# Performance work log

Measured on AMD Instinct MI355X. Metric: run time of the kernel, lower is better.

## Reference

```python
import jax, jax.numpy as jnp
import numpy as np

LEAK = 0.1
BN_EPS = 1e-3  # keras BatchNormalization default epsilon
H = 256        # LSTM hidden size


def _conv1d_same(x, k):
    # x: [B, T, Cin], k: [3, Cin, Cout] -> [B, T, Cout]
    return jax.lax.conv_general_dilated(x, k, (1,), 'SAME',
                                        dimension_numbers=('NWC', 'WIO', 'NWC'))


def _bn_leaky(x, gamma, beta, mean, var):
    y = (x - mean) * jax.lax.rsqrt(var + BN_EPS) * gamma + beta
    return jnp.where(y > 0, y, LEAK * y)


def _lstm_cell(x, h, c, W, U, b):
    # keras LSTMCell: gates ordered i, f, g(candidate), o
    z = x @ W + h @ U + b  # [B, 4H]
    i, f, g, o = jnp.split(z, 4, axis=-1)
    c_new = jax.nn.sigmoid(f) * c + jax.nn.sigmoid(i) * jnp.tanh(g)
    h_new = jax.nn.sigmoid(o) * jnp.tanh(c_new)
    return h_new, c_new


def setup_inputs() -> dict:
    key = jax.random.key(0)
    ks = jax.random.split(key, 16)
    B, T = 128, 1024
    d = {}
    d['imu'] = jax.random.normal(ks[0], (B, T, 6), dtype=jnp.float32)
    # conv encoder params (no bias)
    chans = [(6, 64), (64, 128), (128, 256)]
    for li, (cin, cout) in enumerate(chans, start=1):
        d[f'k{li}'] = jax.random.normal(ks[li], (3, cin, cout), jnp.float32) * (1.0 / np.sqrt(3 * cin))
        d[f'g{li}'] = jnp.ones((cout,), jnp.float32)
        d[f'b{li}'] = jnp.zeros((cout,), jnp.float32)
        d[f'm{li}'] = jax.random.normal(ks[li + 3], (cout,), jnp.float32) * 0.05
        d[f'v{li}'] = jax.random.uniform(ks[li + 6], (cout,), jnp.float32) + 0.5
    # stacked LSTM params (2 layers of 256 units)
    for li, kidx in [(1, 10), (2, 13)]:
        d[f'W{li}'] = jax.random.normal(ks[kidx], (H, 4 * H), jnp.float32) * (1.0 / np.sqrt(H))
        d[f'U{li}'] = jax.random.normal(ks[kidx + 1], (H, 4 * H), jnp.float32) * (1.0 / np.sqrt(H))
        d[f'bl{li}'] = jnp.zeros((4 * H,), jnp.float32)
    return d


def reference(imu, k1, g1, b1, m1, v1, k2, g2, b2, m2, v2, k3, g3, b3, m3, v3,
              W1, U1, bl1, W2, U2, bl2):
    # Conv1D-BN-LeakyReLU encoder (inference-mode BN, training=False)
    x = _bn_leaky(_conv1d_same(imu, k1), g1, b1, m1, v1)
    x = _bn_leaky(_conv1d_same(x, k2), g2, b2, m2, v2)
    x = _bn_leaky(_conv1d_same(x, k3), g3, b3, m3, v3)   # [B, T, 256]

    B = x.shape[0]
    init = tuple(jnp.zeros((B, H), x.dtype) for _ in range(4))  # h1, c1, h2, c2

    def step(carry, xt):
        h1, c1, h2, c2 = carry
        h1, c1 = _lstm_cell(xt, h1, c1, W1, U1, bl1)
        h2, c2 = _lstm_cell(h1, h2, c2, W2, U2, bl2)
        return (h1, c1, h2, c2), h2

    xs = jnp.swapaxes(x, 0, 1)           # [T, B, 256]
    _, ys = jax.lax.scan(step, init, xs)  # ys: [T, B, 256] top-layer outputs
    return jnp.mean(ys, axis=0)           # global average pool over time -> [B, 256]
```

## Files before the change

### kernel.cpp

```cpp
#include <hip/hip_runtime.h>
#include <hip/hip_bf16.h>

#define T_SEQ 1024
#define NB 128
#define HID 256
#define NEGINF_TGT (-(1 << 30))

typedef __attribute__((ext_vector_type(8))) short short8;
typedef __attribute__((ext_vector_type(4))) float f32x4;

__device__ __forceinline__ unsigned short f2bf(float f) {
  unsigned int u = __builtin_bit_cast(unsigned int, f);
  unsigned int r = (u + 0x7fffu + ((u >> 16) & 1u)) >> 16;
  return (unsigned short)r;
}

__device__ __forceinline__ float sigm(float x) { return 1.0f / (1.0f + expf(-x)); }

__device__ __forceinline__ short8 ld_h16(const unsigned short* p) {
  unsigned long long lo = __hip_atomic_load((const unsigned long long*)p,
                                            __ATOMIC_RELAXED, __HIP_MEMORY_SCOPE_AGENT);
  unsigned long long hi = __hip_atomic_load((const unsigned long long*)(p + 4),
                                            __ATOMIC_RELAXED, __HIP_MEMORY_SCOPE_AGENT);
  union { unsigned long long q[2]; short8 v; } u;
  u.q[0] = lo; u.q[1] = hi;
  return u.v;
}
__device__ __forceinline__ void st_h(unsigned short* p, unsigned short v) {
  __hip_atomic_store(p, v, __ATOMIC_RELAXED, __HIP_MEMORY_SCOPE_AGENT);
}

__device__ __forceinline__ void publish(int* tag, int val) {
  asm volatile("s_waitcnt vmcnt(0) lgkmcnt(0)" ::: "memory");
  if (threadIdx.x == 0)
    __hip_atomic_store(tag, val, __ATOMIC_RELAXED, __HIP_MEMORY_SCOPE_AGENT);
}

__device__ __forceinline__ void wait_pair(const int* tags, int tgtA, int tgtB) {
  const int l = threadIdx.x;
  const int* p = tags + (l & 31);
  const int tgt = (l & 16) ? tgtB : tgtA;
  for (;;) {
    int v = __hip_atomic_load(p, __ATOMIC_RELAXED, __HIP_MEMORY_SCOPE_AGENT);
    if (__all(v >= tgt)) break;
  }
  asm volatile("" ::: "memory");
}


__global__ void conv1_kernel(const float* __restrict__ imu, const float* __restrict__ k1,
                             const float* __restrict__ g1, const float* __restrict__ b1,
                             const float* __restrict__ m1, const float* __restrict__ v1,
                             float* __restrict__ y1) {
  int idx = blockIdx.x * 256 + threadIdx.x;
  int c = idx & 63;
  int t = (idx >> 6) & (T_SEQ - 1);
  int b = idx >> 16;
  float acc = 0.f;
#pragma unroll
  for (int dt = 0; dt < 3; ++dt) {
    int tt = t + dt - 1;
    if (tt >= 0 && tt < T_SEQ) {
      const float* ip = imu + ((size_t)b * T_SEQ + tt) * 6;
#pragma unroll
      for (int ci = 0; ci < 6; ++ci)
        acc += ip[ci] * k1[(dt * 6 + ci) * 64 + c];
    }
  }
  float sc = g1[c] * rsqrtf(v1[c] + 1e-3f);
  float y = (acc - m1[c]) * sc + b1[c];
  y1[idx] = y > 0.f ? y : 0.1f * y;
}

__global__ __launch_bounds__(128) void conv2_kernel(
    const float* __restrict__ y1, const float* __restrict__ k2,
    const float* __restrict__ g2, const float* __restrict__ b2,
    const float* __restrict__ m2, const float* __restrict__ v2,
    float* __restrict__ y2) {
  __shared__ float yt[18 * 64];
  const int b = blockIdx.x >> 6;
  const int t0 = (blockIdx.x & 63) << 4;
  for (int i = threadIdx.x; i < 18 * 64; i += 128) {
    int r = i >> 6, ci = i & 63;
    int tt = t0 - 1 + r;
    yt[i] = (tt >= 0 && tt < T_SEQ) ? y1[((size_t)b * T_SEQ + tt) * 64 + ci] : 0.f;
  }
  __syncthreads();
  const int c = threadIdx.x;
  float acc[16];
#pragma unroll
  for (int u = 0; u < 16; ++u) acc[u] = 0.f;
  for (int ci = 0; ci < 64; ++ci) {
    float w0 = k2[(0 * 64 + ci) * 128 + c];
    float w1 = k2[(1 * 64 + ci) * 128 + c];
    float w2 = k2[(2 * 64 + ci) * 128 + c];
    float rv[18];
#pragma unroll
    for (int r = 0; r < 18; ++r) rv[r] = yt[r * 64 + ci];
#pragma unroll
    for (int u = 0; u < 16; ++u)
      acc[u] += rv[u] * w0 + rv[u + 1] * w1 + rv[u + 2] * w2;
  }
  float sc = g2[c] * rsqrtf(v2[c] + 1e-3f);
  float sh = b2[c] - m2[c] * sc;
#pragma unroll
  for (int u = 0; u < 16; ++u) {
    float y = acc[u] * sc + sh;
    y2[((size_t)b * T_SEQ + (t0 + u)) * 128 + c] = y > 0.f ? y : 0.1f * y;
  }
}

__global__ __launch_bounds__(128) void conv3_kernel(
    const float* __restrict__ y2, const float* __restrict__ k3,
    const float* __restrict__ g3, const float* __restrict__ b3,
    const float* __restrict__ m3, const float* __restrict__ v3,
    unsigned short* __restrict__ x) {
  __shared__ float yt[18 * 128];
  const int b = blockIdx.x >> 6;
  const int t0 = (blockIdx.x & 63) << 4;
  for (int i = threadIdx.x; i < 18 * 128; i += 128) {
    int r = i >> 7, ci = i & 127;
    int tt = t0 - 1 + r;
    yt[i] = (tt >= 0 && tt < T_SEQ) ? y2[((size_t)b * T_SEQ + tt) * 128 + ci] : 0.f;
  }
  __syncthreads();
  const int c0 = threadIdx.x;
  float acc0[16], acc1[16];
#pragma unroll
  for (int u = 0; u < 16; ++u) { acc0[u] = 0.f; acc1[u] = 0.f; }
  for (int ci = 0; ci < 128; ++ci) {
    float w00 = k3[(0 * 128 + ci) * 256 + c0];
    float w01 = k3[(1 * 128 + ci) * 256 + c0];
    float w02 = k3[(2 * 128 + ci) * 256 + c0];
    float w10 = k3[(0 * 128 + ci) * 256 + c0 + 128];
    float w11 = k3[(1 * 128 + ci) * 256 + c0 + 128];
    float w12 = k3[(2 * 128 + ci) * 256 + c0 + 128];
    float rv[18];
#pragma unroll
    for (int r = 0; r < 18; ++r) rv[r] = yt[r * 128 + ci];
#pragma unroll
    for (int u = 0; u < 16; ++u) {
      acc0[u] += rv[u] * w00 + rv[u + 1] * w01 + rv[u + 2] * w02;
      acc1[u] += rv[u] * w10 + rv[u + 1] * w11 + rv[u + 2] * w12;
    }
  }
  float sca = g3[c0] * rsqrtf(v3[c0] + 1e-3f);
  float sha = b3[c0] - m3[c0] * sca;
  float scb = g3[c0 + 128] * rsqrtf(v3[c0 + 128] + 1e-3f);
  float shb = b3[c0 + 128] - m3[c0 + 128] * scb;
#pragma unroll
  for (int u = 0; u < 16; ++u) {
    float ya = acc0[u] * sca + sha;
    float yb = acc1[u] * scb + shb;
    ya = ya > 0.f ? ya : 0.1f * ya;
    yb = yb > 0.f ? yb : 0.1f * yb;
    size_t base = ((size_t)(t0 + u) * NB + b) * HID;
    x[base + c0] = f2bf(ya);
    x[base + c0 + 128] = f2bf(yb);
  }
}


__global__ __launch_bounds__(64, 1) void lstm_kernel(
    const unsigned short* __restrict__ x,
    const float* __restrict__ W1, const float* __restrict__ U1, const float* __restrict__ bl1,
    const float* __restrict__ W2, const float* __restrict__ U2, const float* __restrict__ bl2,
    unsigned short* __restrict__ hbufs,
    int* __restrict__ bars,
    float* __restrict__ out) {
  const int team = blockIdx.x >> 5;
  const int bid = blockIdx.x & 31;
  const bool is_l2 = bid >= 16;
  const int pid = bid & 15;
  const int j0 = pid << 4;
  const int lane = threadIdx.x;
  const int b0 = team << 4;

  const float* Wx = is_l2 ? W2 : W1;
  const float* Wh = is_l2 ? U2 : U1;
  const float* bl = is_l2 ? bl2 : bl1;

  const int lo4 = lane & 15;
  const int klo = (lane >> 4) << 3;

  short8 wB[2][8][4];
  {
    const float* Wsrc[2] = {Wx, Wh};
#pragma unroll
    for (int s = 0; s < 2; ++s)
#pragma unroll
      for (int kk = 0; kk < 8; ++kk)
#pragma unroll
        for (int g = 0; g < 4; ++g) {
          short8 v;
#pragma unroll
          for (int e = 0; e < 8; ++e)
            v[e] = (short)f2bf(Wsrc[s][(size_t)(kk * 32 + klo + e) * 1024 + (g << 8) + j0 + lo4]);
          wB[s][kk][g] = v;
        }
  }

  float bias[4];
#pragma unroll
  for (int g = 0; g < 4; ++g) bias[g] = bl[(g << 8) + j0 + lo4];

  unsigned short* h1b = hbufs + (size_t)team * 32768;
  unsigned short* h2b = h1b + 16384;
  int* tags = bars + team * 64;

  const int cbase = ((klo >> 4) << 8) + (lo4 << 4) + (klo & 8);
  const int row = ((lane >> 4) << 2);
  const int stoff = pid * 256 + row * 16 + lo4;

  float cst[4] = {0.f, 0.f, 0.f, 0.f};
  float oacc[4] = {0.f, 0.f, 0.f, 0.f};
  f32x4 acc[4];

  if (!is_l2) {
#pragma unroll
    for (int g = 0; g < 4; ++g) acc[g] = (f32x4){bias[g], bias[g], bias[g], bias[g]};
    {
      const unsigned short* xs = x + (size_t)(b0 + lo4) * HID + klo;
#pragma unroll
      for (int kk = 0; kk < 8; ++kk) {
        short8 a = *(const short8*)(xs + kk * 32);
#pragma unroll
        for (int g = 0; g < 4; ++g)
          acc[g] = __builtin_amdgcn_mfma_f32_16x16x32_bf16(a, wB[0][kk][g], acc[g], 0, 0, 0);
      }
    }

    for (int ph = 0; ph < T_SEQ; ++ph) {
      wait_pair(tags, ph, ph - 3);
      {
        const unsigned short* src = h1b + ((ph + 3) & 3) * 4096 + cbase;
        short8 av[8];
#pragma unroll
        for (int kk = 0; kk < 8; ++kk) av[kk] = ld_h16(src + kk * 512);
#pragma unroll
        for (int kk = 0; kk < 8; ++kk)
#pragma unroll
          for (int g = 0; g < 4; ++g)
            acc[g] = __builtin_amdgcn_mfma_f32_16x16x32_bf16(av[kk], wB[1][kk][g], acc[g], 0, 0, 0);
      }
      unsigned short* dst = h1b + (ph & 3) * 4096 + stoff;
#pragma unroll
      for (int q = 0; q < 4; ++q) {
        float iv = acc[0][q], fv = acc[1][q], gv = acc[2][q], ov = acc[3][q];
        float cn = sigm(fv) * cst[q] + sigm(iv) * tanhf(gv);
        float hn = sigm(ov) * tanhf(cn);
        cst[q] = cn;
        st_h(dst + q * 16, f2bf(hn));
      }
      short8 xv[8];
      if (ph + 1 < T_SEQ) {
        const unsigned short* xs = x + ((size_t)(ph + 1) * NB + b0 + lo4) * HID + klo;
#pragma unroll
        for (int kk = 0; kk < 8; ++kk) xv[kk] = *(const short8*)(xs + kk * 32);
      }
      publish(&tags[pid], ph + 1);
      if (ph + 1 < T_SEQ) {
#pragma unroll
        for (int g = 0; g < 4; ++g) acc[g] = (f32x4){bias[g], bias[g], bias[g], bias[g]};
#pragma unroll
        for (int kk = 0; kk < 8; ++kk)
#pragma unroll
          for (int g = 0; g < 4; ++g)
            acc[g] = __builtin_amdgcn_mfma_f32_16x16x32_bf16(xv[kk], wB[0][kk][g], acc[g], 0, 0, 0);
      }
    }
  } else {
    for (int ph = 0; ph < T_SEQ; ++ph) {
      wait_pair(tags, ph + 1, NEGINF_TGT);
#pragma unroll
      for (int g = 0; g < 4; ++g) acc[g] = (f32x4){bias[g], bias[g], bias[g], bias[g]};
      {
        const unsigned short* s1 = h1b + (ph & 3) * 4096 + cbase;
        short8 av[8];
#pragma unroll
        for (int kk = 0; kk < 8; ++kk) av[kk] = ld_h16(s1 + kk * 512);
#pragma unroll
        for (int kk = 0; kk < 8; ++kk)
#pragma unroll
          for (int g = 0; g < 4; ++g)
            acc[g] = __builtin_amdgcn_mfma_f32_16x16x32_bf16(av[kk], wB[0][kk][g], acc[g], 0, 0, 0);
      }
      wait_pair(tags, NEGINF_TGT, ph);
      {
        const unsigned short* s2 = h2b + ((ph + 3) & 3) * 4096 + cbase;
        short8 av[8];
#pragma unroll
        for (int kk = 0; kk < 8; ++kk) av[kk] = ld_h16(s2 + kk * 512);
#pragma unroll
        for (int kk = 0; kk < 8; ++kk)
#pragma unroll
          for (int g = 0; g < 4; ++g)
            acc[g] = __builtin_amdgcn_mfma_f32_16x16x32_bf16(av[kk], wB[1][kk][g], acc[g], 0, 0, 0);
      }
      unsigned short* dst = h2b + (ph & 3) * 4096 + stoff;
#pragma unroll
      for (int q = 0; q < 4; ++q) {
        float iv = acc[0][q], fv = acc[1][q], gv = acc[2][q], ov = acc[3][q];
        float cn = sigm(fv) * cst[q] + sigm(iv) * tanhf(gv);
        float hn = sigm(ov) * tanhf(cn);
        cst[q] = cn;
        st_h(dst + q * 16, f2bf(hn));
        oacc[q] += hn;
      }
      publish(&tags[16 + pid], ph + 1);
    }
#pragma unroll
    for (int q = 0; q < 4; ++q)
      out[(size_t)(b0 + row + q) * HID + j0 + lo4] = oacc[q] * (1.0f / T_SEQ);
  }
}


extern "C" void kernel_launch(void* const* d_in, const int* in_sizes, int n_in,
                              void* d_out, int out_size, void* d_ws, size_t ws_size,
                              hipStream_t stream) {
  const float* imu = (const float*)d_in[0];
  const float* k1 = (const float*)d_in[1];
  const float* g1 = (const float*)d_in[2];
  const float* b1 = (const float*)d_in[3];
  const float* m1 = (const float*)d_in[4];
  const float* v1 = (const float*)d_in[5];
  const float* k2 = (const float*)d_in[6];
  const float* g2 = (const float*)d_in[7];
  const float* b2 = (const float*)d_in[8];
  const float* m2 = (const float*)d_in[9];
  const float* v2 = (const float*)d_in[10];
  const float* k3 = (const float*)d_in[11];
  const float* g3 = (const float*)d_in[12];
  const float* b3 = (const float*)d_in[13];
  const float* m3 = (const float*)d_in[14];
  const float* v3 = (const float*)d_in[15];
  const float* W1 = (const float*)d_in[16];
  const float* U1 = (const float*)d_in[17];
  const float* bl1 = (const float*)d_in[18];
  const float* W2 = (const float*)d_in[19];
  const float* U2 = (const float*)d_in[20];
  const float* bl2 = (const float*)d_in[21];

  char* ws = (char*)d_ws;
  float* y2 = (float*)ws;
  float* y1 = (float*)(ws + (64u << 20));
  unsigned short* xq = (unsigned short*)(ws + (64u << 20));
  unsigned short* hbufs = (unsigned short*)(ws + (128u << 20));
  int* bars = (int*)(ws + (128u << 20) + (512u << 10));

  hipMemsetAsync(ws + (128u << 20), 0, (512u << 10) + 2048, stream);

  conv1_kernel<<<32768, 256, 0, stream>>>(imu, k1, g1, b1, m1, v1, y1);
  conv2_kernel<<<8192, 128, 0, stream>>>(y1, k2, g2, b2, m2, v2, y2);
  conv3_kernel<<<8192, 128, 0, stream>>>(y2, k3, g3, b3, m3, v3, xq);
  lstm_kernel<<<256, 64, 0, stream>>>(xq, W1, U1, bl1, W2, U2, bl2, hbufs, bars,
                                      (float*)d_out);
}
```

Before: 5.032 ms.

## Group four LSTM wavefronts per block with block-level flags to cut polling

The LSTM kernel now runs 64 blocks of 4 wavefronts instead of 256 single-wave blocks. Each block syncs its waves with __syncthreads and then publishes one padded flag, so every consumer polls 8 cache-line-separated tags instead of 32. This is meant to lower cross-CU flag polling and atomic traffic on each timestep. In exchange every wave in a block must wait for its slowest sibling, and four waves now share one CU's MFMA and VGPR resources.

```diff
diff --git a/kernel.cpp b/kernel.cpp
--- a/kernel.cpp
+++ b/kernel.cpp
@@ -5,6 +5,7 @@
 #define NB 128
 #define HID 256
 #define NEGINF_TGT (-(1 << 30))
+#define TAGSTR 32
 
 typedef __attribute__((ext_vector_type(8))) short short8;
 typedef __attribute__((ext_vector_type(4))) float f32x4;
@@ -30,16 +31,17 @@
   __hip_atomic_store(p, v, __ATOMIC_RELAXED, __HIP_MEMORY_SCOPE_AGENT);
 }
 
-__device__ __forceinline__ void publish(int* tag, int val) {
+__device__ __forceinline__ void publish_block(int* tag, int val) {
   asm volatile("s_waitcnt vmcnt(0) lgkmcnt(0)" ::: "memory");
+  __syncthreads();
   if (threadIdx.x == 0)
     __hip_atomic_store(tag, val, __ATOMIC_RELAXED, __HIP_MEMORY_SCOPE_AGENT);
 }
 
-__device__ __forceinline__ void wait_pair(const int* tags, int tgtA, int tgtB) {
-  const int l = threadIdx.x;
-  const int* p = tags + (l & 31);
-  const int tgt = (l & 16) ? tgtB : tgtA;
+__device__ __forceinline__ void wait_pair(const int* tg, int tgtA, int tgtB) {
+  const int half = (threadIdx.x >> 2) & 1;
+  const int* p = tg + (half * 4 + (threadIdx.x & 3)) * TAGSTR;
+  const int tgt = half ? tgtB : tgtA;
   for (;;) {
     int v = __hip_atomic_load(p, __ATOMIC_RELAXED, __HIP_MEMORY_SCOPE_AGENT);
     if (__all(v >= tgt)) break;
@@ -161,19 +163,21 @@
 }
 
 
-__global__ __launch_bounds__(64, 1) void lstm_kernel(
+__global__ __launch_bounds__(256, 1) void lstm_kernel(
     const unsigned short* __restrict__ x,
     const float* __restrict__ W1, const float* __restrict__ U1, const float* __restrict__ bl1,
     const float* __restrict__ W2, const float* __restrict__ U2, const float* __restrict__ bl2,
     unsigned short* __restrict__ hbufs,
-    int* __restrict__ bars,
+    int* __restrict__ tags,
     float* __restrict__ out) {
-  const int team = blockIdx.x >> 5;
-  const int bid = blockIdx.x & 31;
-  const bool is_l2 = bid >= 16;
-  const int pid = bid & 15;
+  const int team = blockIdx.x >> 3;
+  const int sub = blockIdx.x & 7;
+  const bool is_l2 = sub >= 4;
+  const int bn = sub & 3;
+  const int wv = threadIdx.x >> 6;
+  const int lane = threadIdx.x & 63;
+  const int pid = (bn << 2) + wv;
   const int j0 = pid << 4;
-  const int lane = threadIdx.x;
   const int b0 = team << 4;
 
   const float* Wx = is_l2 ? W2 : W1;
@@ -206,7 +210,7 @@
 
   unsigned short* h1b = hbufs + (size_t)team * 32768;
   unsigned short* h2b = h1b + 16384;
-  int* tags = bars + team * 64;
+  int* tg = tags + team * 8 * TAGSTR;
 
   const int cbase = ((klo >> 4) << 8) + (lo4 << 4) + (klo & 8);
   const int row = ((lane >> 4) << 2);
@@ -231,7 +235,7 @@
     }
 
     for (int ph = 0; ph < T_SEQ; ++ph) {
-      wait_pair(tags, ph, ph - 3);
+      wait_pair(tg, ph, ph - 3);
       {
         const unsigned short* src = h1b + ((ph + 3) & 3) * 4096 + cbase;
         short8 av[8];
@@ -258,7 +262,7 @@
 #pragma unroll
         for (int kk = 0; kk < 8; ++kk) xv[kk] = *(const short8*)(xs + kk * 32);
       }
-      publish(&tags[pid], ph + 1);
+      publish_block(&tg[bn * TAGSTR], ph + 1);
       if (ph + 1 < T_SEQ) {
 #pragma unroll
         for (int g = 0; g < 4; ++g) acc[g] = (f32x4){bias[g], bias[g], bias[g], bias[g]};
@@ -271,7 +275,7 @@
     }
   } else {
     for (int ph = 0; ph < T_SEQ; ++ph) {
-      wait_pair(tags, ph + 1, NEGINF_TGT);
+      wait_pair(tg, ph + 1, NEGINF_TGT);
 #pragma unroll
       for (int g = 0; g < 4; ++g) acc[g] = (f32x4){bias[g], bias[g], bias[g], bias[g]};
       {
@@ -285,7 +289,7 @@
           for (int g = 0; g < 4; ++g)
             acc[g] = __builtin_amdgcn_mfma_f32_16x16x32_bf16(av[kk], wB[0][kk][g], acc[g], 0, 0, 0);
       }
-      wait_pair(tags, NEGINF_TGT, ph);
+      wait_pair(tg, NEGINF_TGT, ph);
       {
         const unsigned short* s2 = h2b + ((ph + 3) & 3) * 4096 + cbase;
         short8 av[8];
@@ -307,7 +311,7 @@
         st_h(dst + q * 16, f2bf(hn));
         oacc[q] += hn;
       }
-      publish(&tags[16 + pid], ph + 1);
+      publish_block(&tg[(4 + bn) * TAGSTR], ph + 1);
     }
 #pragma unroll
     for (int q = 0; q < 4; ++q)
@@ -347,13 +351,13 @@
   float* y1 = (float*)(ws + (64u << 20));
   unsigned short* xq = (unsigned short*)(ws + (64u << 20));
   unsigned short* hbufs = (unsigned short*)(ws + (128u << 20));
-  int* bars = (int*)(ws + (128u << 20) + (512u << 10));
-
-  hipMemsetAsync(ws + (128u << 20), 0, (512u << 10) + 2048, stream);
+  int* tags = (int*)(ws + (128u << 20) + (512u << 10));
+
+  hipMemsetAsync(ws + (128u << 20), 0, (512u << 10) + 8192, stream);
 
   conv1_kernel<<<32768, 256, 0, stream>>>(imu, k1, g1, b1, m1, v1, y1);
   conv2_kernel<<<8192, 128, 0, stream>>>(y1, k2, g2, b2, m2, v2, y2);
   conv3_kernel<<<8192, 128, 0, stream>>>(y2, k3, g3, b3, m3, v3, xq);
-  lstm_kernel<<<256, 64, 0, stream>>>(xq, W1, U1, bl1, W2, U2, bl2, hbufs, bars,
+  lstm_kernel<<<64, 256, 0, stream>>>(xq, W1, U1, bl1, W2, U2, bl2, hbufs, tags,
                                       (float*)d_out);
 }
```

Result: slower. 5.776 ms (+14.8%).

## Replace tag barriers with per-element stamped hidden-state ring polling

Applied to the files above, without the earlier changes.

Each bf16 hidden value is now packed into a 32-bit word with a step stamp in the low half. Consumers poll their fragment directly with cache-bypassing loads until every stamp matches, instead of waiting on separate per-block tags and a publish fence. Layer 1 only throttles on a credit tag that layer-2 blocks write after consuming, and layer 2 pipelines its input-projection MFMA for the next step. The aim is to remove the fence plus tag round trip from the recurrent critical path. The cost is doubled ring traffic, a 16-bit stamp that wraps only past T_SEQ, and reliance on 32-bit store atomicity.

```diff
diff --git a/kernel.cpp b/kernel.cpp
--- a/kernel.cpp
+++ b/kernel.cpp
@@ -4,10 +4,10 @@
 #define T_SEQ 1024
 #define NB 128
 #define HID 256
-#define NEGINF_TGT (-(1 << 30))
 
 typedef __attribute__((ext_vector_type(8))) short short8;
 typedef __attribute__((ext_vector_type(4))) float f32x4;
+typedef __attribute__((ext_vector_type(4))) unsigned int u32x4;
 
 __device__ __forceinline__ unsigned short f2bf(float f) {
   unsigned int u = __builtin_bit_cast(unsigned int, f);
@@ -17,34 +17,59 @@
 
 __device__ __forceinline__ float sigm(float x) { return 1.0f / (1.0f + expf(-x)); }
 
-__device__ __forceinline__ short8 ld_h16(const unsigned short* p) {
-  unsigned long long lo = __hip_atomic_load((const unsigned long long*)p,
-                                            __ATOMIC_RELAXED, __HIP_MEMORY_SCOPE_AGENT);
-  unsigned long long hi = __hip_atomic_load((const unsigned long long*)(p + 4),
-                                            __ATOMIC_RELAXED, __HIP_MEMORY_SCOPE_AGENT);
-  union { unsigned long long q[2]; short8 v; } u;
-  u.q[0] = lo; u.q[1] = hi;
-  return u.v;
-}
-__device__ __forceinline__ void st_h(unsigned short* p, unsigned short v) {
+__device__ __forceinline__ void poll_frag(const unsigned int* base, unsigned int stamp,
+                                          short8 av[8]) {
+  u32x4 t[16];
+  for (;;) {
+    asm volatile(
+        "global_load_dwordx4 %0, %16, off sc0 sc1\n\t"
+        "global_load_dwordx4 %1, %16, off offset:16 sc0 sc1\n\t"
+        "global_load_dwordx4 %2, %16, off offset:128 sc0 sc1\n\t"
+        "global_load_dwordx4 %3, %16, off offset:144 sc0 sc1\n\t"
+        "global_load_dwordx4 %4, %16, off offset:256 sc0 sc1\n\t"
+        "global_load_dwordx4 %5, %16, off offset:272 sc0 sc1\n\t"
+        "global_load_dwordx4 %6, %16, off offset:384 sc0 sc1\n\t"
+        "global_load_dwordx4 %7, %16, off offset:400 sc0 sc1\n\t"
+        "global_load_dwordx4 %8, %16, off offset:512 sc0 sc1\n\t"
+        "global_load_dwordx4 %9, %16, off offset:528 sc0 sc1\n\t"
+        "global_load_dwordx4 %10, %16, off offset:640 sc0 sc1\n\t"
+        "global_load_dwordx4 %11, %16, off offset:656 sc0 sc1\n\t"
+        "global_load_dwordx4 %12, %16, off offset:768 sc0 sc1\n\t"
+        "global_load_dwordx4 %13, %16, off offset:784 sc0 sc1\n\t"
+        "global_load_dwordx4 %14, %16, off offset:896 sc0 sc1\n\t"
+        "global_load_dwordx4 %15, %16, off offset:912 sc0 sc1\n\t"
+        "s_waitcnt vmcnt(0)"
+        : "=&v"(t[0]), "=&v"(t[1]), "=&v"(t[2]), "=&v"(t[3]),
+          "=&v"(t[4]), "=&v"(t[5]), "=&v"(t[6]), "=&v"(t[7]),
+          "=&v"(t[8]), "=&v"(t[9]), "=&v"(t[10]), "=&v"(t[11]),
+          "=&v"(t[12]), "=&v"(t[13]), "=&v"(t[14]), "=&v"(t[15])
+        : "v"(base)
+        : "memory");
+    unsigned int bad = 0;
+#pragma unroll
+    for (int i = 0; i < 16; ++i)
+#pragma unroll
+      for (int e = 0; e < 4; ++e) bad |= (t[i][e] ^ stamp) & 0xffffu;
+    if (__all(bad == 0)) break;
+    __builtin_amdgcn_s_sleep(1);
+  }
+#pragma unroll
+  for (int kk = 0; kk < 8; ++kk) {
+    short8 a;
+#pragma unroll
+    for (int e = 0; e < 4; ++e) {
+      a[e] = (short)(t[2 * kk][e] >> 16);
+      a[4 + e] = (short)(t[2 * kk + 1][e] >> 16);
+    }
+    av[kk] = a;
+  }
+}
+
+__device__ __forceinline__ void st_hw(unsigned int* p, unsigned int v) {
   __hip_atomic_store(p, v, __ATOMIC_RELAXED, __HIP_MEMORY_SCOPE_AGENT);
 }
-
-__device__ __forceinline__ void publish(int* tag, int val) {
-  asm volatile("s_waitcnt vmcnt(0) lgkmcnt(0)" ::: "memory");
-  if (threadIdx.x == 0)
-    __hip_atomic_store(tag, val, __ATOMIC_RELAXED, __HIP_MEMORY_SCOPE_AGENT);
-}
-
-__device__ __forceinline__ void wait_pair(const int* tags, int tgtA, int tgtB) {
-  const int l = threadIdx.x;
-  const int* p = tags + (l & 31);
-  const int tgt = (l & 16) ? tgtB : tgtA;
-  for (;;) {
-    int v = __hip_atomic_load(p, __ATOMIC_RELAXED, __HIP_MEMORY_SCOPE_AGENT);
-    if (__all(v >= tgt)) break;
-  }
-  asm volatile("" ::: "memory");
+__device__ __forceinline__ unsigned int ld_tag(const unsigned int* p) {
+  return __hip_atomic_load(p, __ATOMIC_RELAXED, __HIP_MEMORY_SCOPE_AGENT);
 }
 
 
@@ -165,8 +190,8 @@
     const unsigned short* __restrict__ x,
     const float* __restrict__ W1, const float* __restrict__ U1, const float* __restrict__ bl1,
     const float* __restrict__ W2, const float* __restrict__ U2, const float* __restrict__ bl2,
-    unsigned short* __restrict__ hbufs,
-    int* __restrict__ bars,
+    unsigned int* __restrict__ hrings,
+    unsigned int* __restrict__ tags,
     float* __restrict__ out) {
   const int team = blockIdx.x >> 5;
   const int bid = blockIdx.x & 31;
@@ -204,17 +229,17 @@
 #pragma unroll
   for (int g = 0; g < 4; ++g) bias[g] = bl[(g << 8) + j0 + lo4];
 
-  unsigned short* h1b = hbufs + (size_t)team * 32768;
-  unsigned short* h2b = h1b + 16384;
-  int* tags = bars + team * 64;
-
-  const int cbase = ((klo >> 4) << 8) + (lo4 << 4) + (klo & 8);
+  unsigned int* h1b = hrings + (size_t)team * 32768;
+  unsigned int* h2b = h1b + 16384;
+  unsigned int* ctag = tags + team * 32;
+
+  const int fbase = lo4 * 256 + klo;
   const int row = ((lane >> 4) << 2);
-  const int stoff = pid * 256 + row * 16 + lo4;
 
   float cst[4] = {0.f, 0.f, 0.f, 0.f};
   float oacc[4] = {0.f, 0.f, 0.f, 0.f};
   f32x4 acc[4];
+  short8 av[8];
 
   if (!is_l2) {
 #pragma unroll
@@ -231,35 +256,37 @@
     }
 
     for (int ph = 0; ph < T_SEQ; ++ph) {
-      wait_pair(tags, ph, ph - 3);
-      {
-        const unsigned short* src = h1b + ((ph + 3) & 3) * 4096 + cbase;
-        short8 av[8];
-#pragma unroll
-        for (int kk = 0; kk < 8; ++kk) av[kk] = ld_h16(src + kk * 512);
+      int gv = (int)ld_tag(&ctag[lane & 15]);
+      if (ph > 0) {
+        poll_frag(h1b + ((ph + 3) & 3) * 4096 + fbase, (unsigned)ph, av);
 #pragma unroll
         for (int kk = 0; kk < 8; ++kk)
 #pragma unroll
           for (int g = 0; g < 4; ++g)
             acc[g] = __builtin_amdgcn_mfma_f32_16x16x32_bf16(av[kk], wB[1][kk][g], acc[g], 0, 0, 0);
       }
-      unsigned short* dst = h1b + (ph & 3) * 4096 + stoff;
+      unsigned int stamp = (unsigned)(ph + 1);
+      unsigned int pv[4];
 #pragma unroll
       for (int q = 0; q < 4; ++q) {
-        float iv = acc[0][q], fv = acc[1][q], gv = acc[2][q], ov = acc[3][q];
-        float cn = sigm(fv) * cst[q] + sigm(iv) * tanhf(gv);
+        float iv = acc[0][q], fv = acc[1][q], gg = acc[2][q], ov = acc[3][q];
+        float cn = sigm(fv) * cst[q] + sigm(iv) * tanhf(gg);
         float hn = sigm(ov) * tanhf(cn);
         cst[q] = cn;
-        st_h(dst + q * 16, f2bf(hn));
-      }
-      short8 xv[8];
+        pv[q] = ((unsigned)f2bf(hn) << 16) | stamp;
+      }
+      while (!__all(gv >= ph - 3)) {
+        __builtin_amdgcn_s_sleep(1);
+        gv = (int)ld_tag(&ctag[lane & 15]);
+      }
+      unsigned int* dst = h1b + (ph & 3) * 4096;
+#pragma unroll
+      for (int q = 0; q < 4; ++q) st_hw(dst + (row + q) * 256 + j0 + lo4, pv[q]);
       if (ph + 1 < T_SEQ) {
         const unsigned short* xs = x + ((size_t)(ph + 1) * NB + b0 + lo4) * HID + klo;
+        short8 xv[8];
 #pragma unroll
         for (int kk = 0; kk < 8; ++kk) xv[kk] = *(const short8*)(xs + kk * 32);
-      }
-      publish(&tags[pid], ph + 1);
-      if (ph + 1 < T_SEQ) {
 #pragma unroll
         for (int g = 0; g < 4; ++g) acc[g] = (f32x4){bias[g], bias[g], bias[g], bias[g]};
 #pragma unroll
@@ -270,44 +297,47 @@
       }
     }
   } else {
+    poll_frag(h1b + 0 * 4096 + fbase, 1u, av);
+    if (lane == 0) st_hw(&ctag[pid], 1u);
+#pragma unroll
+    for (int g = 0; g < 4; ++g) acc[g] = (f32x4){bias[g], bias[g], bias[g], bias[g]};
+#pragma unroll
+    for (int kk = 0; kk < 8; ++kk)
+#pragma unroll
+      for (int g = 0; g < 4; ++g)
+        acc[g] = __builtin_amdgcn_mfma_f32_16x16x32_bf16(av[kk], wB[0][kk][g], acc[g], 0, 0, 0);
+
     for (int ph = 0; ph < T_SEQ; ++ph) {
-      wait_pair(tags, ph + 1, NEGINF_TGT);
-#pragma unroll
-      for (int g = 0; g < 4; ++g) acc[g] = (f32x4){bias[g], bias[g], bias[g], bias[g]};
-      {
-        const unsigned short* s1 = h1b + (ph & 3) * 4096 + cbase;
-        short8 av[8];
-#pragma unroll
-        for (int kk = 0; kk < 8; ++kk) av[kk] = ld_h16(s1 + kk * 512);
+      if (ph > 0) {
+        poll_frag(h2b + ((ph + 3) & 3) * 4096 + fbase, (unsigned)ph, av);
+#pragma unroll
+        for (int kk = 0; kk < 8; ++kk)
+#pragma unroll
+          for (int g = 0; g < 4; ++g)
+            acc[g] = __builtin_amdgcn_mfma_f32_16x16x32_bf16(av[kk], wB[1][kk][g], acc[g], 0, 0, 0);
+      }
+      unsigned int stamp = (unsigned)(ph + 1);
+      unsigned int* dst = h2b + (ph & 3) * 4096;
+#pragma unroll
+      for (int q = 0; q < 4; ++q) {
+        float iv = acc[0][q], fv = acc[1][q], gg = acc[2][q], ov = acc[3][q];
+        float cn = sigm(fv) * cst[q] + sigm(iv) * tanhf(gg);
+        float hn = sigm(ov) * tanhf(cn);
+        cst[q] = cn;
+        st_hw(dst + (row + q) * 256 + j0 + lo4, ((unsigned)f2bf(hn) << 16) | stamp);
+        oacc[q] += hn;
+      }
+      if (ph + 1 < T_SEQ) {
+        poll_frag(h1b + ((ph + 1) & 3) * 4096 + fbase, (unsigned)(ph + 2), av);
+        if (lane == 0) st_hw(&ctag[pid], (unsigned)(ph + 2));
+#pragma unroll
+        for (int g = 0; g < 4; ++g) acc[g] = (f32x4){bias[g], bias[g], bias[g], bias[g]};
 #pragma unroll
         for (int kk = 0; kk < 8; ++kk)
 #pragma unroll
           for (int g = 0; g < 4; ++g)
             acc[g] = __builtin_amdgcn_mfma_f32_16x16x32_bf16(av[kk], wB[0][kk][g], acc[g], 0, 0, 0);
       }
-      wait_pair(tags, NEGINF_TGT, ph);
-      {
-        const unsigned short* s2 = h2b + ((ph + 3) & 3) * 4096 + cbase;
-        short8 av[8];
-#pragma unroll
-        for (int kk = 0; kk < 8; ++kk) av[kk] = ld_h16(s2 + kk * 512);
-#pragma unroll
-        for (int kk = 0; kk < 8; ++kk)
-#pragma unroll
-          for (int g = 0; g < 4; ++g)
-            acc[g] = __builtin_amdgcn_mfma_f32_16x16x32_bf16(av[kk], wB[1][kk][g], acc[g], 0, 0, 0);
-      }
-      unsigned short* dst = h2b + (ph & 3) * 4096 + stoff;
-#pragma unroll
-      for (int q = 0; q < 4; ++q) {
-        float iv = acc[0][q], fv = acc[1][q], gv = acc[2][q], ov = acc[3][q];
-        float cn = sigm(fv) * cst[q] + sigm(iv) * tanhf(gv);
-        float hn = sigm(ov) * tanhf(cn);
-        cst[q] = cn;
-        st_h(dst + q * 16, f2bf(hn));
-        oacc[q] += hn;
-      }
-      publish(&tags[16 + pid], ph + 1);
     }
 #pragma unroll
     for (int q = 0; q < 4; ++q)
@@ -346,14 +376,14 @@
   float* y2 = (float*)ws;
   float* y1 = (float*)(ws + (64u << 20));
   unsigned short* xq = (unsigned short*)(ws + (64u << 20));
-  unsigned short* hbufs = (unsigned short*)(ws + (128u << 20));
-  int* bars = (int*)(ws + (128u << 20) + (512u << 10));
-
-  hipMemsetAsync(ws + (128u << 20), 0, (512u << 10) + 2048, stream);
+  unsigned int* hrings = (unsigned int*)(ws + (128u << 20));
+  unsigned int* tags = (unsigned int*)(ws + (128u << 20) + (1u << 20));
+
+  hipMemsetAsync(ws + (128u << 20), 0, (1u << 20) + 1024, stream);
 
   conv1_kernel<<<32768, 256, 0, stream>>>(imu, k1, g1, b1, m1, v1, y1);
   conv2_kernel<<<8192, 128, 0, stream>>>(y1, k2, g2, b2, m2, v2, y2);
   conv3_kernel<<<8192, 128, 0, stream>>>(y2, k3, g3, b3, m3, v3, xq);
-  lstm_kernel<<<256, 64, 0, stream>>>(xq, W1, U1, bl1, W2, U2, bl2, hbufs, bars,
+  lstm_kernel<<<256, 64, 0, stream>>>(xq, W1, U1, bl1, W2, U2, bl2, hrings, tags,
                                       (float*)d_out);
 }
```

New measurement: 5.363 ms. 6.6% more time.
